# Kernel optimization log

Measured on AMD Instinct MI355X. Metric: run time of the kernel, lower is better.

The kernel has to match this reference:

```python
import jax, jax.numpy as jnp
import numpy as np

B, N, CIN, H, E = 1, 20000, 128, 128, 320000


def setup_inputs() -> dict:
    key = jax.random.key(0)
    ks = jax.random.split(key, 16)
    x = jax.random.normal(ks[0], (B, N, CIN), jnp.float32)
    edge_index = jax.random.randint(ks[1], (2, E), 0, N, dtype=jnp.int64)
    edge_weight = jax.random.uniform(ks[2], (E,), jnp.float32)
    h = jax.random.normal(ks[3], (B, N, H), jnp.float32)
    c = jax.random.normal(ks[4], (B, N, H), jnp.float32)
    # GCN stack params, gate order [i, f, c, o]; 2 layers each (K=2)
    Wx0 = jax.random.normal(ks[5], (4, CIN, H), jnp.float32) / np.float32(np.sqrt(CIN))
    bx0 = jnp.zeros((4, H), jnp.float32)
    Wx1 = jax.random.normal(ks[6], (4, H, H), jnp.float32) / np.float32(np.sqrt(H))
    bx1 = jnp.zeros((4, H), jnp.float32)
    Wh0 = jax.random.normal(ks[7], (4, H, H), jnp.float32) / np.float32(np.sqrt(H))
    bh0 = jnp.zeros((4, H), jnp.float32)
    Wh1 = jax.random.normal(ks[8], (4, H, H), jnp.float32) / np.float32(np.sqrt(H))
    bh1 = jnp.zeros((4, H), jnp.float32)
    wc = jax.random.normal(ks[9], (3, H), jnp.float32) * 0.1  # peephole [i, f, o]
    bg = jnp.zeros((4, H), jnp.float32)  # gate biases [i, f, c, o]
    return dict(x=x, edge_index=edge_index, edge_weight=edge_weight, h=h, c=c,
                Wx0=Wx0, bx0=bx0, Wx1=Wx1, bx1=bx1,
                Wh0=Wh0, bh0=bh0, Wh1=Wh1, bh1=bh1, wc=wc, bg=bg)


def reference(x, edge_index, edge_weight, h, c,
              Wx0, bx0, Wx1, bx1, Wh0, bh0, Wh1, bh1, wc, bg):
    n = x.shape[1]
    src, dst = edge_index[0], edge_index[1]
    loop = jnp.arange(n)
    src2 = jnp.concatenate([src, loop])
    dst2 = jnp.concatenate([dst, loop])
    w2 = jnp.concatenate([edge_weight, jnp.ones((n,), edge_weight.dtype)])
    deg = jax.ops.segment_sum(w2, dst2, num_segments=n)
    dis = jnp.where(deg > 0, jax.lax.rsqrt(jnp.maximum(deg, 1e-12)), 0.0)
    norm = dis[src2] * w2 * dis[dst2]  # sym GCN norm with self loops

    def prop(t):  # t: [..., N, F] -> D^-1/2 (A+I) D^-1/2 t
        lead = t.shape[:-2]
        tf = t.reshape((-1,) + t.shape[-2:])
        m = tf[:, src2, :] * norm[None, :, None]
        agg = jax.vmap(lambda mm: jax.ops.segment_sum(mm, dst2, num_segments=n))(m)
        return agg.reshape(lead + agg.shape[-2:])

    def gcn4(t, W0, b0, W1, b1):  # 2-layer GCN, 4 gates at once
        a = prop(t)  # shared first aggregation: [B,N,F]
        h0 = jax.nn.relu(jnp.einsum('bnc,gch->gbnh', a, W0) + b0[:, None, None, :])
        a1 = prop(h0)  # [4,B,N,H]
        return jnp.einsum('gbnh,ghk->gbnk', a1, W1) + b1[:, None, None, :]

    G = gcn4(x, Wx0, bx0, Wx1, bx1) + gcn4(h, Wh0, bh0, Wh1, bh1)  # [4,B,N,H]
    I = jax.nn.sigmoid(G[0] + wc[0] * c + bg[0])
    F = jax.nn.sigmoid(G[1] + wc[1] * c + bg[1])
    T = jnp.tanh(G[2] + bg[2])
    Cn = F * c + I * T
    O = jax.nn.sigmoid(G[3] + wc[2] * Cn + bg[3])
    Hn = O * jnp.tanh(Cn)
    return (Hn, Cn)
```

## Files before the change

### kernel.cpp

```cpp
#include <hip/hip_runtime.h>
#include <hip/hip_bf16.h>
#include <stdint.h>

#define NN    20000
#define NP    20096
#define EE    320000
#define CH    128
#define GC    512
#define NHtot 2560000

typedef short bf16x8 __attribute__((ext_vector_type(8)));
typedef float f32x4  __attribute__((ext_vector_type(4)));

__device__ __forceinline__ unsigned short f2bf(float f) {
    __hip_bfloat16 b = __float2bfloat16(f);
    union { __hip_bfloat16 b; unsigned short u; } c; c.b = b; return c.u;
}
__device__ __forceinline__ void fma4(uint2 u, float n, float* acc) {
    union { unsigned int i; float f; } t;
    t.i = u.x << 16;         acc[0] += n * t.f;
    t.i = u.x & 0xffff0000u; acc[1] += n * t.f;
    t.i = u.y << 16;         acc[2] += n * t.f;
    t.i = u.y & 0xffff0000u; acc[3] += n * t.f;
}
__device__ __forceinline__ void tof4(uint2 u, float* f) {
    union { unsigned int i; float f; } t;
    t.i = u.x << 16;         f[0] = t.f;
    t.i = u.x & 0xffff0000u; f[1] = t.f;
    t.i = u.y << 16;         f[2] = t.f;
    t.i = u.y & 0xffff0000u; f[3] = t.f;
}
__device__ __forceinline__ uint2 pack4(const float* f) {
    uint2 v;
    v.x = (unsigned int)f2bf(f[0]) | ((unsigned int)f2bf(f[1]) << 16);
    v.y = (unsigned int)f2bf(f[2]) | ((unsigned int)f2bf(f[3]) << 16);
    return v;
}
__device__ __forceinline__ void gload_lds16(const void* g, void* l) {
    __builtin_amdgcn_global_load_lds(
        (const __attribute__((address_space(1))) void*)g,
        (__attribute__((address_space(3))) void*)l, 16, 0, 0);
}

__global__ void k_cntprep(const int* __restrict__ ei, int* __restrict__ cnt,
                          const float* __restrict__ W0, const float* __restrict__ W1,
                          const float* __restrict__ W2, const float* __restrict__ W3,
                          unsigned short* __restrict__ T0, unsigned short* __restrict__ T1,
                          unsigned short* __restrict__ T2, unsigned short* __restrict__ T3,
                          const float* __restrict__ bx1, const float* __restrict__ bh1,
                          const float* __restrict__ bg, float* __restrict__ btot) {
    int bid = blockIdx.x;
    if (bid < EE / 256) {
        int e = bid * 256 + threadIdx.x;
        atomicAdd(&cnt[ei[EE + e]], 1);
        return;
    }
    int pid = bid - EE / 256;
    int z = pid >> 8, y = (pid >> 6) & 3, xb = pid & 63;
    if (z == 0 && y == 0 && xb < 2) {
        int f = xb * 256 + threadIdx.x;
        btot[f] = bx1[f] + bh1[f] + bg[f];
    }
    const float* W; unsigned short* T;
    switch (z) {
        case 0:  W = W0; T = T0; break;
        case 1:  W = W1; T = T1; break;
        case 2:  W = W2; T = T2; break;
        default: W = W3; T = T3; break;
    }
    int n = xb * 2 + (threadIdx.x >> 7);
    int k = threadIdx.x & 127;
    T[((size_t)y * 128 + n) * 128 + k] = f2bf(W[((size_t)y * 128 + k) * 128 + n]);
}

__global__ void k_scan1(const int* __restrict__ cnt, int* __restrict__ rowoff,
                        int* __restrict__ bsum) {
    __shared__ int wsum[4];
    int i = blockIdx.x * 256 + threadIdx.x;
    int self = (i < NN) ? cnt[i] : 0;
    int lane = threadIdx.x & 63, wid = threadIdx.x >> 6;
    int v = self;
    #pragma unroll
    for (int off = 1; off < 64; off <<= 1) {
        int u = __shfl_up(v, off);
        if (lane >= off) v += u;
    }
    if (lane == 63) wsum[wid] = v;
    __syncthreads();
    int wof = 0;
    for (int k = 0; k < wid; ++k) wof += wsum[k];
    if (i < NN) rowoff[i] = wof + v - self;
    if (threadIdx.x == 255) bsum[blockIdx.x] = wof + v;
}

__global__ void k_scan2(int* __restrict__ bsum) {
    int lane = threadIdx.x;
    int base = 0;
    for (int start = 0; start < 80; start += 64) {
        int i = start + lane;
        int self = (i < 80) ? bsum[i] : 0;
        int v = self;
        #pragma unroll
        for (int off = 1; off < 64; off <<= 1) {
            int u = __shfl_up(v, off);
            if (lane >= off) v += u;
        }
        if (i < 80) bsum[i] = base + v - self;
        base += __shfl(v, 63);
    }
}

__global__ void k_scan3(int* __restrict__ rowoff, const int* __restrict__ bsum,
                        int* __restrict__ cur) {
    int i = blockIdx.x * 256 + threadIdx.x;
    if (i < NN) {
        int v = rowoff[i] + bsum[i >> 8];
        rowoff[i] = v; cur[i] = v;
    }
    if (i == NN) rowoff[NN] = EE;
}

__global__ void k_scatter(const int* __restrict__ ei, const float* __restrict__ ew,
                          int* __restrict__ cur,
                          int* __restrict__ csrs, float* __restrict__ csrw) {
    int e = blockIdx.x * 256 + threadIdx.x;
    if (e >= EE) return;
    int s = ei[e], d = ei[EE + e];
    int p = atomicAdd(&cur[d], 1);
    csrs[p] = s; csrw[p] = ew[e];
}

__global__ __launch_bounds__(256) void k_degcast(
        const float* __restrict__ x, const float* __restrict__ h,
        const int* __restrict__ rowoff, const float* __restrict__ csrw,
        float* __restrict__ dis, unsigned short* __restrict__ xhb) {
    int wid = threadIdx.x >> 6, lane = threadIdx.x & 63;
    int w = blockIdx.x * 4 + wid;
    int e0 = rowoff[w], e1 = rowoff[w + 1];
    float s = 0.f;
    for (int e = e0 + lane; e < e1; e += 64) s += csrw[e];
    #pragma unroll
    for (int off = 32; off; off >>= 1) s += __shfl_xor(s, off);
    float dn = rsqrtf(fmaxf(1.0f + s, 1e-12f));
    if (lane == 0) dis[w] = dn;
    const float* src = (lane < 32) ? x + (size_t)w * CH + lane * 4
                                   : h + (size_t)w * CH + (lane - 32) * 4;
    float4 v = *(const float4*)src;
    float f[4] = { dn * v.x, dn * v.y, dn * v.z, dn * v.w };
    *(uint2*)(xhb + (size_t)w * 256 + lane * 4) = pack4(f);
}

__global__ __launch_bounds__(128) void k_prop256(
        const unsigned short* __restrict__ tab, unsigned short* __restrict__ o,
        const int* __restrict__ rowoff, const int* __restrict__ csrs,
        const float* __restrict__ csrw, const float* __restrict__ dis) {
    int w = blockIdx.x * 2 + (threadIdx.x >> 6);
    int lane = threadIdx.x & 63;
    const uint2* T2 = (const uint2*)tab;
    float acc[4];
    tof4(T2[(size_t)w * 64 + lane], acc);
    int e = rowoff[w], e1 = rowoff[w + 1];
    for (; e + 8 <= e1; e += 8) {
        int   s0 = csrs[e],   s1 = csrs[e+1], s2 = csrs[e+2], s3 = csrs[e+3];
        int   s4 = csrs[e+4], s5 = csrs[e+5], s6 = csrs[e+6], s7 = csrs[e+7];
        uint2 u0 = T2[(size_t)s0 * 64 + lane];
        uint2 u1 = T2[(size_t)s1 * 64 + lane];
        uint2 u2 = T2[(size_t)s2 * 64 + lane];
        uint2 u3 = T2[(size_t)s3 * 64 + lane];
        uint2 u4 = T2[(size_t)s4 * 64 + lane];
        uint2 u5 = T2[(size_t)s5 * 64 + lane];
        uint2 u6 = T2[(size_t)s6 * 64 + lane];
        uint2 u7 = T2[(size_t)s7 * 64 + lane];
        float n0 = csrw[e],   n1 = csrw[e+1], n2 = csrw[e+2], n3 = csrw[e+3];
        float n4 = csrw[e+4], n5 = csrw[e+5], n6 = csrw[e+6], n7 = csrw[e+7];
        fma4(u0, n0, acc); fma4(u1, n1, acc); fma4(u2, n2, acc); fma4(u3, n3, acc);
        fma4(u4, n4, acc); fma4(u5, n5, acc); fma4(u6, n6, acc); fma4(u7, n7, acc);
    }
    for (; e + 4 <= e1; e += 4) {
        int   s0 = csrs[e],   s1 = csrs[e+1], s2 = csrs[e+2], s3 = csrs[e+3];
        float n0 = csrw[e],   n1 = csrw[e+1], n2 = csrw[e+2], n3 = csrw[e+3];
        uint2 u0 = T2[(size_t)s0 * 64 + lane];
        uint2 u1 = T2[(size_t)s1 * 64 + lane];
        uint2 u2 = T2[(size_t)s2 * 64 + lane];
        uint2 u3 = T2[(size_t)s3 * 64 + lane];
        fma4(u0, n0, acc); fma4(u1, n1, acc); fma4(u2, n2, acc); fma4(u3, n3, acc);
    }
    for (; e < e1; ++e) {
        fma4(T2[(size_t)csrs[e] * 64 + lane], csrw[e], acc);
    }
    float dw = dis[w];
    #pragma unroll
    for (int j = 0; j < 4; ++j) acc[j] *= dw;
    ((uint2*)o)[(size_t)w * 64 + lane] = pack4(acc);
}

#define SWZ(r, c8) (((r) << 4) + ((c8) ^ ((r) & 15)))

__global__ __launch_bounds__(256) void k_gemm1(
        const unsigned short* __restrict__ A,
        const unsigned short* __restrict__ Wtx, const unsigned short* __restrict__ Wth,
        const float* __restrict__ bx0, const float* __restrict__ bh0,
        unsigned short* __restrict__ outx, unsigned short* __restrict__ outh) {
    __shared__ uint4 As[2048];
    __shared__ uint4 Bs[2048];
    const int side = blockIdx.z;
    const int aoff = side * 128;
    const unsigned short* Wt = side ? Wth : Wtx;
    const float* bias        = side ? bh0 : bx0;
    unsigned short* out      = side ? outh : outx;

    const int    g    = blockIdx.y;
    const size_t row0 = (size_t)blockIdx.x * 128;
    const int    t    = threadIdx.x;
    const int    wv   = t >> 6;
    const unsigned short* Wg = Wt + (size_t)g * 16384;

    #pragma unroll
    for (int p = 0; p < 8; ++p) {
        int id = t + 256 * p, r = id >> 4, cc = id & 15;
        int c8 = cc ^ (r & 15);
        gload_lds16(A + (row0 + r) * 256 + aoff + c8 * 8, &As[p * 256 + wv * 64]);
        gload_lds16(Wg + r * CH + c8 * 8,                 &Bs[p * 256 + wv * 64]);
    }
    __syncthreads();

    const int l = t & 63;
    const int m0 = (wv >> 1) * 64, n0 = (wv & 1) * 64;
    const int lm = l & 15, q = l >> 4;
    f32x4 acc[4][4];
    #pragma unroll
    for (int i = 0; i < 4; ++i)
        #pragma unroll
        for (int j = 0; j < 4; ++j) { acc[i][j][0]=0.f; acc[i][j][1]=0.f; acc[i][j][2]=0.f; acc[i][j][3]=0.f; }

    #pragma unroll
    for (int kc = 0; kc < 4; ++kc) {
        int c8 = kc * 4 + q;
        bf16x8 a[4], b[4];
        #pragma unroll
        for (int i = 0; i < 4; ++i) { int r = m0 + i * 16 + lm; a[i] = *(const bf16x8*)&As[SWZ(r, c8)]; }
        #pragma unroll
        for (int j = 0; j < 4; ++j) { int r = n0 + j * 16 + lm; b[j] = *(const bf16x8*)&Bs[SWZ(r, c8)]; }
        #pragma unroll
        for (int i = 0; i < 4; ++i)
            #pragma unroll
            for (int j = 0; j < 4; ++j)
                acc[i][j] = __builtin_amdgcn_mfma_f32_16x16x32_bf16(a[i], b[j], acc[i][j], 0, 0, 0);
    }

    #pragma unroll
    for (int j = 0; j < 4; ++j) {
        float bb = bias[g * CH + n0 + j * 16 + lm];
        #pragma unroll
        for (int i = 0; i < 4; ++i)
            #pragma unroll
            for (int r = 0; r < 4; ++r) {
                int rowl = m0 + i * 16 + q * 4 + r;
                int col  = n0 + j * 16 + lm;
                out[(row0 + rowl) * GC + g * CH + col] = f2bf(fmaxf(acc[i][j][r] + bb, 0.f));
            }
    }
}

__global__ __launch_bounds__(256) void k_gemm2(
        const unsigned short* __restrict__ A1, const unsigned short* __restrict__ A2,
        const unsigned short* __restrict__ Wt1, const unsigned short* __restrict__ Wt2,
        const float* __restrict__ dis, unsigned short* __restrict__ outS) {
    __shared__ uint4 As[2048];
    __shared__ uint4 Bs[2048];
    const int    g    = blockIdx.y;
    const size_t row0 = (size_t)blockIdx.x * 128;
    const int    t    = threadIdx.x;
    const int    wv   = t >> 6;
    const int l = t & 63;
    const int m0 = (wv >> 1) * 64, n0 = (wv & 1) * 64;
    const int lm = l & 15, q = l >> 4;
    f32x4 acc[4][4];
    #pragma unroll
    for (int i = 0; i < 4; ++i)
        #pragma unroll
        for (int j = 0; j < 4; ++j) { acc[i][j][0]=0.f; acc[i][j][1]=0.f; acc[i][j][2]=0.f; acc[i][j][3]=0.f; }

    for (int side = 0; side < 2; ++side) {
        if (side) __syncthreads();
        const unsigned short* Ap = side ? A2 : A1;
        const unsigned short* Wg = (side ? Wt2 : Wt1) + (size_t)g * 16384;
        #pragma unroll
        for (int p = 0; p < 8; ++p) {
            int id = t + 256 * p, r = id >> 4, cc = id & 15;
            int c8 = cc ^ (r & 15);
            gload_lds16(Ap + (row0 + r) * GC + g * CH + c8 * 8, &As[p * 256 + wv * 64]);
            gload_lds16(Wg + r * CH + c8 * 8,                   &Bs[p * 256 + wv * 64]);
        }
        __syncthreads();
        #pragma unroll
        for (int kc = 0; kc < 4; ++kc) {
            int c8 = kc * 4 + q;
            bf16x8 a[4], b[4];
            #pragma unroll
            for (int i = 0; i < 4; ++i) { int r = m0 + i * 16 + lm; a[i] = *(const bf16x8*)&As[SWZ(r, c8)]; }
            #pragma unroll
            for (int j = 0; j < 4; ++j) { int r = n0 + j * 16 + lm; b[j] = *(const bf16x8*)&Bs[SWZ(r, c8)]; }
            #pragma unroll
            for (int i = 0; i < 4; ++i)
                #pragma unroll
                for (int j = 0; j < 4; ++j)
                    acc[i][j] = __builtin_amdgcn_mfma_f32_16x16x32_bf16(a[i], b[j], acc[i][j], 0, 0, 0);
        }
    }

    #pragma unroll
    for (int j = 0; j < 4; ++j)
        #pragma unroll
        for (int i = 0; i < 4; ++i)
            #pragma unroll
            for (int r = 0; r < 4; ++r) {
                int rowl = m0 + i * 16 + q * 4 + r;
                int col  = n0 + j * 16 + lm;
                float dr = dis[row0 + rowl];
                outS[(row0 + rowl) * GC + g * CH + col] = f2bf(dr * acc[i][j][r]);
            }
}

#define GIDX(f) ((f) + ((f) >> 5))
__global__ __launch_bounds__(128) void k_prop512g(
        const unsigned short* __restrict__ Sb, float* __restrict__ out,
        const int* __restrict__ rowoff, const int* __restrict__ csrs,
        const float* __restrict__ csrw, const float* __restrict__ dis,
        const float* __restrict__ c, const float* __restrict__ btot,
        const float* __restrict__ wc) {
    __shared__ float gbuf[528];
    int half = threadIdx.x >> 6, lane = threadIdx.x & 63;
    int w = blockIdx.x;
    const uint2* S2 = (const uint2*)Sb;
    size_t foff = (size_t)half * 64 + lane;
    float acc[4];
    tof4(S2[(size_t)w * 128 + foff], acc);
    int e = rowoff[w], e1 = rowoff[w + 1];
    for (; e + 8 <= e1; e += 8) {
        int   s0 = csrs[e],   s1 = csrs[e+1], s2 = csrs[e+2], s3 = csrs[e+3];
        int   s4 = csrs[e+4], s5 = csrs[e+5], s6 = csrs[e+6], s7 = csrs[e+7];
        uint2 u0 = S2[(size_t)s0 * 128 + foff];
        uint2 u1 = S2[(size_t)s1 * 128 + foff];
        uint2 u2 = S2[(size_t)s2 * 128 + foff];
        uint2 u3 = S2[(size_t)s3 * 128 + foff];
        uint2 u4 = S2[(size_t)s4 * 128 + foff];
        uint2 u5 = S2[(size_t)s5 * 128 + foff];
        uint2 u6 = S2[(size_t)s6 * 128 + foff];
        uint2 u7 = S2[(size_t)s7 * 128 + foff];
        float n0 = csrw[e],   n1 = csrw[e+1], n2 = csrw[e+2], n3 = csrw[e+3];
        float n4 = csrw[e+4], n5 = csrw[e+5], n6 = csrw[e+6], n7 = csrw[e+7];
        fma4(u0, n0, acc); fma4(u1, n1, acc); fma4(u2, n2, acc); fma4(u3, n3, acc);
        fma4(u4, n4, acc); fma4(u5, n5, acc); fma4(u6, n6, acc); fma4(u7, n7, acc);
    }
    for (; e + 4 <= e1; e += 4) {
        int   s0 = csrs[e],   s1 = csrs[e+1], s2 = csrs[e+2], s3 = csrs[e+3];
        float n0 = csrw[e],   n1 = csrw[e+1], n2 = csrw[e+2], n3 = csrw[e+3];
        uint2 u0 = S2[(size_t)s0 * 128 + foff];
        uint2 u1 = S2[(size_t)s1 * 128 + foff];
        uint2 u2 = S2[(size_t)s2 * 128 + foff];
        uint2 u3 = S2[(size_t)s3 * 128 + foff];
        fma4(u0, n0, acc); fma4(u1, n1, acc); fma4(u2, n2, acc); fma4(u3, n3, acc);
    }
    for (; e < e1; ++e) {
        fma4(S2[(size_t)csrs[e] * 128 + foff], csrw[e], acc);
    }
    float dw = dis[w];
    #pragma unroll
    for (int j = 0; j < 4; ++j) {
        int f = half * 256 + lane * 4 + j;
        gbuf[GIDX(f)] = dw * acc[j];
    }
    __syncthreads();
    int hh = threadIdx.x;
    float g0 = gbuf[GIDX(hh)]       + btot[hh];
    float g1 = gbuf[GIDX(128 + hh)] + btot[128 + hh];
    float g2 = gbuf[GIDX(256 + hh)] + btot[256 + hh];
    float g3 = gbuf[GIDX(384 + hh)] + btot[384 + hh];
    float cv = c[(size_t)w * CH + hh];
    float I  = 1.f / (1.f + expf(-(g0 + wc[hh]       * cv)));
    float F  = 1.f / (1.f + expf(-(g1 + wc[128 + hh] * cv)));
    float T  = tanhf(g2);
    float Cn = F * cv + I * T;
    float O  = 1.f / (1.f + expf(-(g3 + wc[256 + hh] * Cn)));
    out[(size_t)w * CH + hh]         = O * tanhf(Cn);
    out[NHtot + (size_t)w * CH + hh] = Cn;
}

extern "C" void kernel_launch(void* const* d_in, const int* in_sizes, int n_in,
                              void* d_out, int out_size, void* d_ws, size_t ws_size,
                              hipStream_t stream) {
    (void)in_sizes; (void)n_in; (void)out_size; (void)ws_size;
    const float* x   = (const float*)d_in[0];
    const int*   ei  = (const int*)d_in[1];
    const float* ew  = (const float*)d_in[2];
    const float* h   = (const float*)d_in[3];
    const float* c   = (const float*)d_in[4];
    const float* Wx0 = (const float*)d_in[5];
    const float* bx0 = (const float*)d_in[6];
    const float* Wx1 = (const float*)d_in[7];
    const float* bx1 = (const float*)d_in[8];
    const float* Wh0 = (const float*)d_in[9];
    const float* bh0 = (const float*)d_in[10];
    const float* Wh1 = (const float*)d_in[11];
    const float* bh1 = (const float*)d_in[12];
    const float* wc  = (const float*)d_in[13];
    const float* bg  = (const float*)d_in[14];
    float* out = (float*)d_out;

    float* wsf  = (float*)d_ws;
    float* dis  = wsf;
    int*   cnt  = (int*)(wsf + 20480);
    int*   row  = (int*)(wsf + 40960);
    int*   cur  = (int*)(wsf + 61696);
    int*   bsum = (int*)(wsf + 82176);
    float* btot = wsf + 82432;
    int*   csrs = (int*)(wsf + 82944);
    float* csrw = wsf + 402944;
    unsigned short* Wt0x = (unsigned short*)(wsf + 722944);
    unsigned short* Wt0h = (unsigned short*)(wsf + 755712);
    unsigned short* Wt1x = (unsigned short*)(wsf + 788480);
    unsigned short* Wt1h = (unsigned short*)(wsf + 821248);
    unsigned short* xhb  = (unsigned short*)(wsf + 854016);
    unsigned short* axh  = (unsigned short*)(wsf + 3426304);
    unsigned short* h0x  = (unsigned short*)(wsf + 5998592);
    unsigned short* h0h  = (unsigned short*)(wsf + 11143168);
    unsigned short* Sb   = (unsigned short*)(wsf + 16287744);

    hipMemsetAsync(cnt, 0, 20480 * sizeof(int), stream);

    k_cntprep<<<EE / 256 + 1024, 256, 0, stream>>>(ei, cnt,
                                                   Wx0, Wh0, Wx1, Wh1,
                                                   Wt0x, Wt0h, Wt1x, Wt1h,
                                                   bx1, bh1, bg, btot);
    k_scan1  <<<80, 256, 0, stream>>>(cnt, row, bsum);
    k_scan2  <<<1, 64, 0, stream>>>(bsum);
    k_scan3  <<<80, 256, 0, stream>>>(row, bsum, cur);
    k_scatter<<<EE / 256, 256, 0, stream>>>(ei, ew, cur, csrs, csrw);

    k_degcast<<<NN / 4, 256, 0, stream>>>(x, h, row, csrw, dis, xhb);

    k_prop256<<<NN / 2, 128, 0, stream>>>(xhb, axh, row, csrs, csrw, dis);

    dim3 g1(NP / 128, 4, 2);
    k_gemm1<<<g1, 256, 0, stream>>>(axh, Wt0x, Wt0h, bx0, bh0, h0x, h0h);
    dim3 g2(NP / 128, 4);
    k_gemm2<<<g2, 256, 0, stream>>>(h0x, h0h, Wt1x, Wt1h, dis, Sb);

    k_prop512g<<<NN, 128, 0, stream>>>(Sb, out, row, csrs, csrw, dis, c, btot, wc);
}
```

Measured before the change: 252.5 us.

## Interleave gate columns and split final propagation into feature chunks per wave

The second GEMM now writes its output with the four gates interleaved in 16-column groups, and the bias vector is permuted to match. The final propagate-plus-LSTM kernel is replaced by one where each wave handles a 64-column chunk of four nodes, so each lane gathers one bf16 per edge. The gates are combined with cross-lane shuffles instead of a shared-memory round trip and barrier. The aim is to spread the gather over more, smaller blocks and drop the LDS exchange, at the cost of 2-byte loads per lane (128 bytes per wave per edge) and reading the CSR index and weight arrays eight times per node.

```diff
diff --git a/kernel.cpp b/kernel.cpp
--- a/kernel.cpp
+++ b/kernel.cpp
@@ -29,6 +29,10 @@
     t.i = u.x & 0xffff0000u; f[1] = t.f;
     t.i = u.y << 16;         f[2] = t.f;
     t.i = u.y & 0xffff0000u; f[3] = t.f;
+}
+__device__ __forceinline__ float bfu(unsigned short u) {
+    union { unsigned int i; float f; } t;
+    t.i = (unsigned int)u << 16; return t.f;
 }
 __device__ __forceinline__ uint2 pack4(const float* f) {
     uint2 v;
@@ -59,7 +63,9 @@
     int z = pid >> 8, y = (pid >> 6) & 3, xb = pid & 63;
     if (z == 0 && y == 0 && xb < 2) {
         int f = xb * 256 + threadIdx.x;
-        btot[f] = bx1[f] + bh1[f] + bg[f];
+        int g = f >> 7, hh = f & 127;
+        int pos = ((hh >> 4) << 6) | (g << 4) | (hh & 15);
+        btot[pos] = bx1[f] + bh1[f] + bg[f];
     }
     const float* W; unsigned short* T;
     switch (z) {
@@ -310,81 +316,75 @@
     }
 
     #pragma unroll
-    for (int j = 0; j < 4; ++j)
+    for (int j = 0; j < 4; ++j) {
+        int fh = (n0 + j * 16) >> 4;
         #pragma unroll
         for (int i = 0; i < 4; ++i)
             #pragma unroll
             for (int r = 0; r < 4; ++r) {
                 int rowl = m0 + i * 16 + q * 4 + r;
-                int col  = n0 + j * 16 + lm;
                 float dr = dis[row0 + rowl];
-                outS[(row0 + rowl) * GC + g * CH + col] = f2bf(dr * acc[i][j][r]);
+                outS[(row0 + rowl) * GC + fh * 64 + g * 16 + lm] = f2bf(dr * acc[i][j][r]);
             }
-}
-
-#define GIDX(f) ((f) + ((f) >> 5))
-__global__ __launch_bounds__(128) void k_prop512g(
+    }
+}
+
+__global__ __launch_bounds__(256) void k_prop512c(
         const unsigned short* __restrict__ Sb, float* __restrict__ out,
         const int* __restrict__ rowoff, const int* __restrict__ csrs,
         const float* __restrict__ csrw, const float* __restrict__ dis,
         const float* __restrict__ c, const float* __restrict__ btot,
         const float* __restrict__ wc) {
-    __shared__ float gbuf[528];
-    int half = threadIdx.x >> 6, lane = threadIdx.x & 63;
-    int w = blockIdx.x;
-    const uint2* S2 = (const uint2*)Sb;
-    size_t foff = (size_t)half * 64 + lane;
-    float acc[4];
-    tof4(S2[(size_t)w * 128 + foff], acc);
+    int chunk = blockIdx.x & 7;
+    int w = (blockIdx.x >> 3) * 4 + (threadIdx.x >> 6);
+    int l = threadIdx.x & 63;
+    const unsigned short* Sp = Sb + (size_t)chunk * 64 + l;
+    float acc = bfu(Sp[(size_t)w * GC]);
     int e = rowoff[w], e1 = rowoff[w + 1];
     for (; e + 8 <= e1; e += 8) {
-        int   s0 = csrs[e],   s1 = csrs[e+1], s2 = csrs[e+2], s3 = csrs[e+3];
-        int   s4 = csrs[e+4], s5 = csrs[e+5], s6 = csrs[e+6], s7 = csrs[e+7];
-        uint2 u0 = S2[(size_t)s0 * 128 + foff];
-        uint2 u1 = S2[(size_t)s1 * 128 + foff];
-        uint2 u2 = S2[(size_t)s2 * 128 + foff];
-        uint2 u3 = S2[(size_t)s3 * 128 + foff];
-        uint2 u4 = S2[(size_t)s4 * 128 + foff];
-        uint2 u5 = S2[(size_t)s5 * 128 + foff];
-        uint2 u6 = S2[(size_t)s6 * 128 + foff];
-        uint2 u7 = S2[(size_t)s7 * 128 + foff];
+        int s0 = csrs[e],   s1 = csrs[e+1], s2 = csrs[e+2], s3 = csrs[e+3];
+        int s4 = csrs[e+4], s5 = csrs[e+5], s6 = csrs[e+6], s7 = csrs[e+7];
+        unsigned short u0 = Sp[(size_t)s0 * GC];
+        unsigned short u1 = Sp[(size_t)s1 * GC];
+        unsigned short u2 = Sp[(size_t)s2 * GC];
+        unsigned short u3 = Sp[(size_t)s3 * GC];
+        unsigned short u4 = Sp[(size_t)s4 * GC];
+        unsigned short u5 = Sp[(size_t)s5 * GC];
+        unsigned short u6 = Sp[(size_t)s6 * GC];
+        unsigned short u7 = Sp[(size_t)s7 * GC];
         float n0 = csrw[e],   n1 = csrw[e+1], n2 = csrw[e+2], n3 = csrw[e+3];
         float n4 = csrw[e+4], n5 = csrw[e+5], n6 = csrw[e+6], n7 = csrw[e+7];
-        fma4(u0, n0, acc); fma4(u1, n1, acc); fma4(u2, n2, acc); fma4(u3, n3, acc);
-        fma4(u4, n4, acc); fma4(u5, n5, acc); fma4(u6, n6, acc); fma4(u7, n7, acc);
+        acc += n0 * bfu(u0); acc += n1 * bfu(u1); acc += n2 * bfu(u2); acc += n3 * bfu(u3);
+        acc += n4 * bfu(u4); acc += n5 * bfu(u5); acc += n6 * bfu(u6); acc += n7 * bfu(u7);
     }
     for (; e + 4 <= e1; e += 4) {
-        int   s0 = csrs[e],   s1 = csrs[e+1], s2 = csrs[e+2], s3 = csrs[e+3];
+        int s0 = csrs[e],   s1 = csrs[e+1], s2 = csrs[e+2], s3 = csrs[e+3];
+        unsigned short u0 = Sp[(size_t)s0 * GC];
+        unsigned short u1 = Sp[(size_t)s1 * GC];
+        unsigned short u2 = Sp[(size_t)s2 * GC];
+        unsigned short u3 = Sp[(size_t)s3 * GC];
         float n0 = csrw[e],   n1 = csrw[e+1], n2 = csrw[e+2], n3 = csrw[e+3];
-        uint2 u0 = S2[(size_t)s0 * 128 + foff];
-        uint2 u1 = S2[(size_t)s1 * 128 + foff];
-        uint2 u2 = S2[(size_t)s2 * 128 + foff];
-        uint2 u3 = S2[(size_t)s3 * 128 + foff];
-        fma4(u0, n0, acc); fma4(u1, n1, acc); fma4(u2, n2, acc); fma4(u3, n3, acc);
+        acc += n0 * bfu(u0); acc += n1 * bfu(u1); acc += n2 * bfu(u2); acc += n3 * bfu(u3);
     }
     for (; e < e1; ++e) {
-        fma4(S2[(size_t)csrs[e] * 128 + foff], csrw[e], acc);
+        acc += csrw[e] * bfu(Sp[(size_t)csrs[e] * GC]);
     }
     float dw = dis[w];
-    #pragma unroll
-    for (int j = 0; j < 4; ++j) {
-        int f = half * 256 + lane * 4 + j;
-        gbuf[GIDX(f)] = dw * acc[j];
-    }
-    __syncthreads();
-    int hh = threadIdx.x;
-    float g0 = gbuf[GIDX(hh)]       + btot[hh];
-    float g1 = gbuf[GIDX(128 + hh)] + btot[128 + hh];
-    float g2 = gbuf[GIDX(256 + hh)] + btot[256 + hh];
-    float g3 = gbuf[GIDX(384 + hh)] + btot[384 + hh];
-    float cv = c[(size_t)w * CH + hh];
-    float I  = 1.f / (1.f + expf(-(g0 + wc[hh]       * cv)));
-    float F  = 1.f / (1.f + expf(-(g1 + wc[128 + hh] * cv)));
-    float T  = tanhf(g2);
-    float Cn = F * cv + I * T;
-    float O  = 1.f / (1.f + expf(-(g3 + wc[256 + hh] * Cn)));
-    out[(size_t)w * CH + hh]         = O * tanhf(Cn);
-    out[NHtot + (size_t)w * CH + hh] = Cn;
+    float v  = dw * acc + btot[chunk * 64 + l];
+    float x1 = __shfl_xor(v, 16);
+    float x2 = __shfl_xor(v, 32);
+    float x3 = __shfl_xor(v, 48);
+    if ((l >> 4) == 0) {
+        int hh = chunk * 16 + (l & 15);
+        float cv = c[(size_t)w * CH + hh];
+        float I  = 1.f / (1.f + expf(-(v  + wc[hh]       * cv)));
+        float F  = 1.f / (1.f + expf(-(x1 + wc[128 + hh] * cv)));
+        float T  = tanhf(x2);
+        float Cn = F * cv + I * T;
+        float O  = 1.f / (1.f + expf(-(x3 + wc[256 + hh] * Cn)));
+        out[(size_t)w * CH + hh]         = O * tanhf(Cn);
+        out[NHtot + (size_t)w * CH + hh] = Cn;
+    }
 }
 
 extern "C" void kernel_launch(void* const* d_in, const int* in_sizes, int n_in,
@@ -447,5 +447,5 @@
     dim3 g2(NP / 128, 4);
     k_gemm2<<<g2, 256, 0, stream>>>(h0x, h0h, Wt1x, Wt1h, dis, Sb);
 
-    k_prop512g<<<NN, 128, 0, stream>>>(Sb, out, row, csrs, csrw, dis, c, btot, wc);
-}
+    k_prop512c<<<(NN / 4) * 8, 256, 0, stream>>>(Sb, out, row, csrs, csrw, dis, c, btot, wc);
+}
```

Result: slower. 305.7 us (+21.1%).
